# Kernel tuning notes

Measured on AMD Instinct MI355X. Metric: run time of the kernel, lower is better.

Reference implementation:

```python
import jax, jax.numpy as jnp
import numpy as np

N_QUBITS = 10
N_LAYERS = 2
BATCH = 4096


def _apply_1q(state, U, w):
    """Apply a single-qubit gate U ((2,2) or (batch,2,2)) on wire w.
    state: (batch, 2,2,...,2) with axis w+1 for wire w (wire 0 = leftmost)."""
    s = jnp.moveaxis(state, w + 1, -1)
    if U.ndim == 2:
        s = jnp.einsum('ij,...j->...i', U, s)
    else:  # per-sample gate (AngleEmbedding)
        s = jnp.einsum('bij,b...j->b...i', U, s)
    return jnp.moveaxis(s, -1, w + 1)


def _apply_cnot(state, c, t):
    ax_c, ax_t = c + 1, t + 1
    s0 = jnp.take(state, jnp.array([0]), axis=ax_c)
    s1 = jnp.take(state, jnp.array([1]), axis=ax_c)
    s1 = jnp.flip(s1, axis=ax_t)  # X on target where control == 1
    return jnp.concatenate([s0, s1], axis=ax_c)


def _ry(theta):
    """RY gate; theta scalar -> (2,2), theta (batch,) -> (batch,2,2)."""
    c, s = jnp.cos(theta / 2), jnp.sin(theta / 2)
    return jnp.stack([jnp.stack([c, -s], -1), jnp.stack([s, c], -1)], -2).astype(jnp.complex64)


def _rot(phi, theta, omega):
    """PennyLane Rot(phi, theta, omega) = RZ(omega) @ RY(theta) @ RZ(phi)."""
    c, s = jnp.cos(theta / 2), jnp.sin(theta / 2)
    ep = jnp.exp(-0.5j * (phi + omega))
    em = jnp.exp(0.5j * (phi - omega))
    return jnp.stack([
        jnp.stack([ep * c, -em * s], -1),
        jnp.stack([jnp.conj(em) * s, jnp.conj(ep) * c], -1),
    ], -2).astype(jnp.complex64)


def _qcircuit(x, weights):
    batch, n = x.shape
    L = weights.shape[0]
    state = jnp.zeros((batch,) + (2,) * n, dtype=jnp.complex64)
    state = state.at[(slice(None),) + (0,) * n].set(1.0)
    # AngleEmbedding, rotation='Y'
    for w in range(n):
        state = _apply_1q(state, _ry(x[:, w]), w)
    # StronglyEntanglingLayers: Rot on each wire, then CNOT ring with range r
    for l in range(L):
        for w in range(n):
            state = _apply_1q(state, _rot(weights[l, w, 0], weights[l, w, 1], weights[l, w, 2]), w)
        r = (l % (n - 1)) + 1
        for w in range(n):
            state = _apply_cnot(state, w, (w + r) % n)
    probs = state.real ** 2 + state.imag ** 2
    zs = []
    for w in range(n):
        axes = tuple(a for a in range(1, n + 1) if a != w + 1)
        m = probs.sum(axis=axes)  # (batch, 2)
        zs.append(m[:, 0] - m[:, 1])  # <Z_w>
    return jnp.stack(zs, axis=1).astype(jnp.float32)  # (batch, n)


def setup_inputs() -> dict:
    key = jax.random.key(0)
    ks = jax.random.split(key, 6)
    x = jax.random.uniform(ks[0], (BATCH, N_QUBITS), dtype=jnp.float32, maxval=2 * np.pi)
    weights = jax.random.uniform(ks[1], (N_LAYERS, N_QUBITS, 3), dtype=jnp.float32, maxval=2 * np.pi)
    w1 = jax.random.normal(ks[2], (8, N_QUBITS), dtype=jnp.float32) * 0.3
    b1 = jax.random.normal(ks[3], (8,), dtype=jnp.float32) * 0.1
    w2 = jax.random.normal(ks[4], (1, 8), dtype=jnp.float32) * 0.3
    b2 = jax.random.normal(ks[5], (1,), dtype=jnp.float32) * 0.1
    return {"x": x, "weights": weights, "w1": w1, "b1": b1, "w2": w2, "b2": b2}


def reference(x, weights, w1, b1, w2, b2):
    q = _qcircuit(x, weights)                 # (batch, n_qubits)
    h = jax.nn.relu(q @ w1.T + b1)            # (batch, 8)
    return jax.nn.sigmoid(h @ w2.T + b2)      # (batch, 1)
```

## Files before the change

kernel.cpp:

```cpp
#include <hip/hip_runtime.h>
#include <math.h>

#define NQ 10
#define BATCH 4096


struct CR { int c, t, flip; };
__host__ __device__ constexpr CR cnot_conj(int lc, int lt) {
    const int xc = lc & 1, zc = (lc >> 1) & 1;
    const int xt = lt & 1, zt = (lt >> 1) & 1;
    const int flip = xc & zt & ((xt ^ zc) ^ 1);
    const int nxt = xt ^ xc;
    const int nzc = zc ^ zt;
    return { (nzc << 1) | xc, (zt << 1) | nxt, flip };
}

template<int SM, int K, int L1, int L0, int F>
__device__ __forceinline__ float chain(const float (&B)[NQ][4], const float (&C)[NQ][4], float p) {
    if constexpr (K == 0) {
        constexpr CR r = cnot_conj(L0, L1);
        float v = p;
        if constexpr (r.t != 0) v *= B[1][r.t];
        if constexpr (r.c != 0) v *= B[0][r.c];
        if constexpr (F ^ r.flip) return -v; else return v;
    } else if constexpr ((SM >> K) & 1) {
        float s = 0.f;
        {   constexpr CR r = cnot_conj(1, L1);
            float p2 = p * C[K][1];
            if constexpr (r.t != 0) p2 *= B[K + 1][r.t];
            s += chain<SM, K - 1, r.c, L0, F ^ r.flip>(B, C, p2); }
        {   constexpr CR r = cnot_conj(2, L1);
            float p2 = p * C[K][2];
            if constexpr (r.t != 0) p2 *= B[K + 1][r.t];
            s += chain<SM, K - 1, r.c, L0, F ^ r.flip>(B, C, p2); }
        {   constexpr CR r = cnot_conj(3, L1);
            float p2 = p * C[K][3];
            if constexpr (r.t != 0) p2 *= B[K + 1][r.t];
            s += chain<SM, K - 1, r.c, L0, F ^ r.flip>(B, C, p2); }
        return s;
    } else {
        constexpr CR r = cnot_conj(0, L1);
        float p2 = p;
        if constexpr (r.t != 0) p2 *= B[K + 1][r.t];
        return chain<SM, K - 1, r.c, L0, F ^ r.flip>(B, C, p2);
    }
}

template<int SM, int S0, int S9>
__device__ __forceinline__ float top2(const float (&B)[NQ][4], const float (&C)[NQ][4]) {
    constexpr CR r = cnot_conj(S9, S0);
    float p = 1.f;
    if constexpr (S0 != 0) p *= C[0][S0];
    if constexpr (S9 != 0) p *= C[9][S9];
    return chain<SM, 8, r.c, r.t, r.flip>(B, C, p);
}
template<int SM, int S0>
__device__ __forceinline__ float sum9(const float (&B)[NQ][4], const float (&C)[NQ][4]) {
    if constexpr ((SM >> 9) & 1)
        return top2<SM, S0, 1>(B, C) + top2<SM, S0, 2>(B, C) + top2<SM, S0, 3>(B, C);
    else
        return top2<SM, S0, 0>(B, C);
}
template<int SM>
__device__ __forceinline__ float obs_eval(const float (&B)[NQ][4], const float (&C)[NQ][4]) {
    if constexpr (SM & 1)
        return sum9<SM, 1>(B, C) + sum9<SM, 2>(B, C) + sum9<SM, 3>(B, C);
    else
        return sum9<SM, 0>(B, C);
}

__global__ void precompute(const float* __restrict__ weights, float* __restrict__ ws) {
    int w = threadIdx.x;
    if (w >= NQ) return;
    float phi0 = weights[w * 3 + 0], th0 = weights[w * 3 + 1], om0 = weights[w * 3 + 2];
    float phi1 = weights[(NQ + w) * 3 + 0], th1 = weights[(NQ + w) * 3 + 1];
    float cp, sp_, co, so, ct, st;
    sincosf(phi0, &sp_, &cp);
    sincosf(th0,  &st,  &ct);
    sincosf(om0,  &so,  &co);
    ws[w * 6 + 0] = co * ct * cp - so * sp_;
    ws[w * 6 + 1] = so * ct * cp + co * sp_;
    ws[w * 6 + 2] = -st * cp;
    ws[w * 6 + 3] = co * st;
    ws[w * 6 + 4] = so * st;
    ws[w * 6 + 5] = ct;
    float c1p, s1p, c1t, s1t;
    sincosf(phi1, &s1p, &c1p);
    sincosf(th1,  &s1t, &c1t);
    ws[120 + w] = -s1t * c1p;
    ws[130 + w] =  c1t;
    ws[140 + w] =  s1t * s1p;
}

__global__ __launch_bounds__(64) void qnn_kernel(
    const float* __restrict__ x, const float* __restrict__ ws,
    const float* __restrict__ w1, const float* __restrict__ b1,
    const float* __restrict__ w2, const float* __restrict__ b2,
    float* __restrict__ out)
{
    const int s = blockIdx.x * 64 + threadIdx.x;

    float B[NQ][4];
    float C[NQ][4];
    const float2* xp = (const float2*)(x + s * NQ);
    #pragma unroll
    for (int h = 0; h < 5; ++h) {
        float2 xv = xp[h];
        #pragma unroll
        for (int g = 0; g < 2; ++g) {
            int w = 2 * h + g;
            float sx, cx;
            sincosf(g ? xv.y : xv.x, &sx, &cx);
            const float* q = ws + w * 6;
            B[w][0] = 1.f;
            B[w][1] = fmaf(sx, q[0], cx * q[3]);
            B[w][3] = fmaf(sx, q[1], cx * q[4]);
            B[w][2] = fmaf(sx, q[2], cx * q[5]);
            C[w][0] = 1.f;
            C[w][1] = ws[120 + w];
            C[w][2] = ws[130 + w];
            C[w][3] = ws[140 + w];
        }
    }

    float z[NQ];
    z[0] = obs_eval<0x154>(B, C);
    z[1] = obs_eval<0x2A8>(B, C);
    z[2] = obs_eval<0x005>(B, C);
    z[3] = obs_eval<0x00A>(B, C);
    z[4] = obs_eval<0x015>(B, C);
    z[5] = obs_eval<0x02A>(B, C);
    z[6] = obs_eval<0x055>(B, C);
    z[7] = obs_eval<0x0AA>(B, C);
    z[8] = obs_eval<0x155>(B, C);
    z[9] = obs_eval<0x2AA>(B, C);

    float acc2 = b2[0];
    #pragma unroll
    for (int j = 0; j < 8; ++j) {
        float h = b1[j];
        #pragma unroll
        for (int w = 0; w < NQ; ++w)
            h = fmaf(z[w], w1[j * NQ + w], h);
        h = fmaxf(h, 0.f);
        acc2 = fmaf(h, w2[j], acc2);
    }
    out[s] = 1.f / (1.f + expf(-acc2));
}

extern "C" void kernel_launch(void* const* d_in, const int* in_sizes, int n_in,
                              void* d_out, int out_size, void* d_ws, size_t ws_size,
                              hipStream_t stream) {
    const float* x       = (const float*)d_in[0];
    const float* weights = (const float*)d_in[1];
    const float* w1      = (const float*)d_in[2];
    const float* b1      = (const float*)d_in[3];
    const float* w2      = (const float*)d_in[4];
    const float* b2      = (const float*)d_in[5];
    float* out = (float*)d_out;
    float* ws  = (float*)d_ws;

    precompute<<<1, 64, 0, stream>>>(weights, ws);
    qnn_kernel<<<BATCH / 64, 64, 0, stream>>>(x, ws, w1, b1, w2, b2, out);
}
```

Before: 74.35 us.

## Fuse weight precompute into main kernel and split observables across four wavefronts

```diff
diff --git a/kernel.cpp b/kernel.cpp
--- a/kernel.cpp
+++ b/kernel.cpp
@@ -69,83 +69,100 @@
         return sum9<SM, 0>(B, C);
 }
 
-__global__ void precompute(const float* __restrict__ weights, float* __restrict__ ws) {
-    int w = threadIdx.x;
-    if (w >= NQ) return;
-    float phi0 = weights[w * 3 + 0], th0 = weights[w * 3 + 1], om0 = weights[w * 3 + 2];
-    float phi1 = weights[(NQ + w) * 3 + 0], th1 = weights[(NQ + w) * 3 + 1];
-    float cp, sp_, co, so, ct, st;
-    sincosf(phi0, &sp_, &cp);
-    sincosf(th0,  &st,  &ct);
-    sincosf(om0,  &so,  &co);
-    ws[w * 6 + 0] = co * ct * cp - so * sp_;
-    ws[w * 6 + 1] = so * ct * cp + co * sp_;
-    ws[w * 6 + 2] = -st * cp;
-    ws[w * 6 + 3] = co * st;
-    ws[w * 6 + 4] = so * st;
-    ws[w * 6 + 5] = ct;
-    float c1p, s1p, c1t, s1t;
-    sincosf(phi1, &s1p, &c1p);
-    sincosf(th1,  &s1t, &c1t);
-    ws[120 + w] = -s1t * c1p;
-    ws[130 + w] =  c1t;
-    ws[140 + w] =  s1t * s1p;
-}
-
-__global__ __launch_bounds__(64) void qnn_kernel(
-    const float* __restrict__ x, const float* __restrict__ ws,
+__global__ __launch_bounds__(256) void qnn_kernel(
+    const float* __restrict__ x, const float* __restrict__ weights,
     const float* __restrict__ w1, const float* __restrict__ b1,
     const float* __restrict__ w2, const float* __restrict__ b2,
     float* __restrict__ out)
 {
-    const int s = blockIdx.x * 64 + threadIdx.x;
+    __shared__ float U[60];
+    __shared__ float CCs[40];
+    __shared__ float zb[64 * 11];
+
+    const int t = threadIdx.x;
+
+    if (t < NQ) {
+        float phi0 = weights[t * 3 + 0], th0 = weights[t * 3 + 1], om0 = weights[t * 3 + 2];
+        float phi1 = weights[(NQ + t) * 3 + 0], th1 = weights[(NQ + t) * 3 + 1];
+        float cp, sp_, co, so, ct, st;
+        sincosf(phi0, &sp_, &cp);
+        sincosf(th0,  &st,  &ct);
+        sincosf(om0,  &so,  &co);
+        U[t * 6 + 0] = co * ct * cp - so * sp_;
+        U[t * 6 + 1] = so * ct * cp + co * sp_;
+        U[t * 6 + 2] = -st * cp;
+        U[t * 6 + 3] = co * st;
+        U[t * 6 + 4] = so * st;
+        U[t * 6 + 5] = ct;
+        float c1p, s1p, c1t, s1t;
+        sincosf(phi1, &s1p, &c1p);
+        sincosf(th1,  &s1t, &c1t);
+        CCs[t * 4 + 1] = -s1t * c1p;
+        CCs[t * 4 + 2] =  c1t;
+        CCs[t * 4 + 3] =  s1t * s1p;
+    }
+    __syncthreads();
+
+    const int g    = t >> 6;
+    const int lane = t & 63;
+    const int sample = blockIdx.x * 64 + lane;
 
     float B[NQ][4];
     float C[NQ][4];
-    const float2* xp = (const float2*)(x + s * NQ);
+    const float2* xp = (const float2*)(x + sample * NQ);
     #pragma unroll
     for (int h = 0; h < 5; ++h) {
         float2 xv = xp[h];
         #pragma unroll
-        for (int g = 0; g < 2; ++g) {
-            int w = 2 * h + g;
+        for (int q2 = 0; q2 < 2; ++q2) {
+            int w = 2 * h + q2;
             float sx, cx;
-            sincosf(g ? xv.y : xv.x, &sx, &cx);
-            const float* q = ws + w * 6;
+            __sincosf(q2 ? xv.y : xv.x, &sx, &cx);
             B[w][0] = 1.f;
-            B[w][1] = fmaf(sx, q[0], cx * q[3]);
-            B[w][3] = fmaf(sx, q[1], cx * q[4]);
-            B[w][2] = fmaf(sx, q[2], cx * q[5]);
+            B[w][1] = fmaf(sx, U[w * 6 + 0], cx * U[w * 6 + 3]);
+            B[w][3] = fmaf(sx, U[w * 6 + 1], cx * U[w * 6 + 4]);
+            B[w][2] = fmaf(sx, U[w * 6 + 2], cx * U[w * 6 + 5]);
             C[w][0] = 1.f;
-            C[w][1] = ws[120 + w];
-            C[w][2] = ws[130 + w];
-            C[w][3] = ws[140 + w];
+            C[w][1] = CCs[w * 4 + 1];
+            C[w][2] = CCs[w * 4 + 2];
+            C[w][3] = CCs[w * 4 + 3];
         }
     }
 
-    float z[NQ];
-    z[0] = obs_eval<0x154>(B, C);
-    z[1] = obs_eval<0x2A8>(B, C);
-    z[2] = obs_eval<0x005>(B, C);
-    z[3] = obs_eval<0x00A>(B, C);
-    z[4] = obs_eval<0x015>(B, C);
-    z[5] = obs_eval<0x02A>(B, C);
-    z[6] = obs_eval<0x055>(B, C);
-    z[7] = obs_eval<0x0AA>(B, C);
-    z[8] = obs_eval<0x155>(B, C);
-    z[9] = obs_eval<0x2AA>(B, C);
+    float* zrow = zb + lane * 11;
+    if (g == 0) {
+        zrow[8] = obs_eval<0x155>(B, C);
+        zrow[2] = obs_eval<0x005>(B, C);
+    } else if (g == 1) {
+        zrow[9] = obs_eval<0x2AA>(B, C);
+        zrow[3] = obs_eval<0x00A>(B, C);
+    } else if (g == 2) {
+        zrow[0] = obs_eval<0x154>(B, C);
+        zrow[6] = obs_eval<0x055>(B, C);
+        zrow[4] = obs_eval<0x015>(B, C);
+    } else {
+        zrow[1] = obs_eval<0x2A8>(B, C);
+        zrow[7] = obs_eval<0x0AA>(B, C);
+        zrow[5] = obs_eval<0x02A>(B, C);
+    }
+    __syncthreads();
 
-    float acc2 = b2[0];
-    #pragma unroll
-    for (int j = 0; j < 8; ++j) {
-        float h = b1[j];
+    if (g == 0) {
+        float z[NQ];
         #pragma unroll
-        for (int w = 0; w < NQ; ++w)
-            h = fmaf(z[w], w1[j * NQ + w], h);
-        h = fmaxf(h, 0.f);
-        acc2 = fmaf(h, w2[j], acc2);
+        for (int w = 0; w < NQ; ++w) z[w] = zb[lane * 11 + w];
+        float acc2 = b2[0];
+        #pragma unroll
+        for (int j = 0; j < 8; ++j) {
+            float h = b1[j];
+            #pragma unroll
+            for (int w = 0; w < NQ; ++w)
+                h = fmaf(z[w], w1[j * NQ + w], h);
+            h = fmaxf(h, 0.f);
+            acc2 = fmaf(h, w2[j], acc2);
+        }
+        out[sample] = 1.f / (1.f + __expf(-acc2));
     }
-    out[s] = 1.f / (1.f + expf(-acc2));
 }
 
 extern "C" void kernel_launch(void* const* d_in, const int* in_sizes, int n_in,
@@ -158,8 +175,6 @@
     const float* w2      = (const float*)d_in[4];
     const float* b2      = (const float*)d_in[5];
     float* out = (float*)d_out;
-    float* ws  = (float*)d_ws;
 
-    precompute<<<1, 64, 0, stream>>>(weights, ws);
-    qnn_kernel<<<BATCH / 64, 64, 0, stream>>>(x, ws, w1, b1, w2, b2, out);
+    qnn_kernel<<<BATCH / 64, 256, 0, stream>>>(x, weights, w1, b1, w2, b2, out);
 }
```

Result: faster. 67.84 us (-8.8%).
